# Performance work log

Hardware: AMD Instinct MI355X
Metric: run time of the kernel (lower is better)

## Reference

```python
import jax, jax.numpy as jnp
import numpy as np

N, K, C = 128, 64, 64

def _w(key, shape, scale):
    return (jax.random.normal(key, shape, dtype=jnp.float32) * scale)

def setup_inputs() -> dict:
    key = jax.random.key(0)
    ks = jax.random.split(key, 20)
    s1 = 1.0 / np.sqrt(C)
    s2 = 1.0 / np.sqrt(2 * C)
    inp = {
        "x": jax.random.normal(ks[0], (N, K, C), dtype=jnp.float32),
        "W_lin": _w(ks[1], (C, C), s1), "b_lin": jnp.zeros((C,), jnp.float32),
        # unary_passing: Linear(C,C) -> tanh -> Linear(C,C)
        "Wu1": _w(ks[2], (C, C), s1), "bu1": jnp.zeros((C,), jnp.float32),
        "Wu2": _w(ks[3], (C, C), s1), "bu2": jnp.zeros((C,), jnp.float32),
        # unary_gate: Linear(C,C) -> tanh -> Linear(C,C) -> sigmoid
        "Wug1": _w(ks[4], (C, C), s1), "bug1": jnp.zeros((C,), jnp.float32),
        "Wug2": _w(ks[5], (C, C), s1), "bug2": jnp.zeros((C,), jnp.float32),
        # binary_passing: Linear(2C,C) -> tanh -> Linear(C,C)
        "Wb1": _w(ks[6], (2 * C, C), s2), "bb1": jnp.zeros((C,), jnp.float32),
        "Wb2": _w(ks[7], (C, C), s1), "bb2": jnp.zeros((C,), jnp.float32),
        # binary_gate: Linear(2C,C) -> tanh -> Linear(C,C) -> sigmoid
        "Wbg1": _w(ks[8], (2 * C, C), s2), "bbg1": jnp.zeros((C,), jnp.float32),
        "Wbg2": _w(ks[9], (C, C), s1), "bbg2": jnp.zeros((C,), jnp.float32),
        "t": 0,  # time scalar, ignored by IgnoreLinear base layer
    }
    return inp


def reference(x, W_lin, b_lin, Wu1, bu1, Wu2, bu2, Wug1, bug1, Wug2, bug2,
              Wb1, bb1, Wb2, bb2, Wbg1, bbg1, Wbg2, bbg2, t):
    # base linear map (IgnoreLinear: ignores t)
    h = x @ W_lin + b_lin                          # (N, K, C)
    n, k, c = h.shape
    # unary message with gate
    um = jnp.tanh(h @ Wu1 + bu1) @ Wu2 + bu2
    ug = jax.nn.sigmoid(jnp.tanh(h @ Wug1 + bug1) @ Wug2 + bug2)
    um = um * ug                                   # (N, K, C)
    # all-pairs broadcast-concat: hm[n,i,j] = [h[n,j], h[n,i]]
    hm = jnp.concatenate([
        jnp.broadcast_to(h[:, None, :, :], (n, k, k, c)),
        jnp.broadcast_to(h[:, :, None, :], (n, k, k, c)),
    ], axis=3)                                     # (N, K, K, 2C)
    bm = jnp.tanh(hm @ Wb1 + bb1) @ Wb2 + bb2      # (N, K, K, C)
    bg = jax.nn.sigmoid(jnp.tanh(hm @ Wbg1 + bbg1) @ Wbg2 + bbg2)
    # sum over axis 1 (includes diagonal, as in original), normalize by K-1
    bm = jnp.sum(bm * bg, axis=1) / jnp.float32(k - 1)  # (N, K, C)
    return um + bm
```

## Files before the change

kernel.cpp:

```cpp
#include <hip/hip_runtime.h>

#define WST 72
#define LOG2E 1.44269504f

typedef __attribute__((ext_vector_type(4))) float    f32x4;
typedef __attribute__((ext_vector_type(2))) float    f32x2;
typedef __attribute__((ext_vector_type(8))) _Float16 f16x8;
typedef __attribute__((ext_vector_type(2))) _Float16 f16x2;
typedef __attribute__((ext_vector_type(2))) __fp16   fp16x2_raw;

union U8 { f16x8 v; f16x2 h[4]; };

__device__ __forceinline__ float rcp_f(float x) { return __builtin_amdgcn_rcpf(x); }
__device__ __forceinline__ float exp2_f(float x) { return __builtin_amdgcn_exp2f(x); }
__device__ __forceinline__ float fast_sigmoid(float x) {
    return rcp_f(1.0f + __expf(-x));
}
__device__ __forceinline__ float tanh_exp(float x) {
    return 1.0f - 2.0f * rcp_f(__expf(2.0f * x) + 1.0f);
}
__device__ __forceinline__ f16x2 pkrtz(float a, float b) {
    fp16x2_raw r = __builtin_amdgcn_cvt_pkrtz(a, b);
    return __builtin_bit_cast(f16x2, r);
}

__device__ __forceinline__ void wload8(const float* __restrict__ W, int tid, float v[8]) {
#pragma unroll
    for (int i = 0; i < 8; ++i) v[i] = W[tid + i * 512];
}
__device__ __forceinline__ void wstore8(_Float16* Wt, int tid, const float v[8], float scale) {
#pragma unroll
    for (int i = 0; i < 8; ++i) {
        int idx = tid + i * 512;
        Wt[(idx & 63) * WST + (idx >> 6)] = (_Float16)(v[i] * scale);
    }
}
__device__ __forceinline__ void wload16(const float* __restrict__ W, int t256, float v[16]) {
#pragma unroll
    for (int i = 0; i < 16; ++i) v[i] = W[t256 + i * 256];
}

__device__ __forceinline__ void gemm2(const _Float16* Act, int arow, int qd,
                                      const _Float16* Wt, int colb,
                                      f32x4 acc[2]) {
    f16x8 a0 = *(const f16x8*)(Act + arow * WST + qd * 8);
    f16x8 a1 = *(const f16x8*)(Act + arow * WST + 32 + qd * 8);
#pragma unroll
    for (int cc = 0; cc < 2; ++cc) {
        const _Float16* wr = Wt + (colb + cc * 16) * WST + qd * 8;
        f16x8 b0 = *(const f16x8*)(wr);
        f16x8 b1 = *(const f16x8*)(wr + 32);
        acc[cc] = __builtin_amdgcn_mfma_f32_16x16x32_f16(a0, b0, acc[cc], 0, 0, 0);
        acc[cc] = __builtin_amdgcn_mfma_f32_16x16x32_f16(a1, b1, acc[cc], 0, 0, 0);
    }
}

__global__ __launch_bounds__(512, 2) void fused_all_kernel(
    const float* __restrict__ x,
    const float* __restrict__ W_lin, const float* __restrict__ b_lin,
    const float* __restrict__ Wu1,  const float* __restrict__ bu1,
    const float* __restrict__ Wu2,  const float* __restrict__ bu2,
    const float* __restrict__ Wug1, const float* __restrict__ bug1,
    const float* __restrict__ Wug2, const float* __restrict__ bug2,
    const float* __restrict__ Wb1,  const float* __restrict__ bb1,
    const float* __restrict__ Wb2,  const float* __restrict__ bb2,
    const float* __restrict__ Wbg1, const float* __restrict__ bbg1,
    const float* __restrict__ Wbg2, const float* __restrict__ bbg2,
    float* __restrict__ out)
{
    __shared__ __align__(16) char smem[152576];
    _Float16* WLs = (_Float16*)(smem);
    _Float16* SX  = (_Float16*)(smem + 9216);
    _Float16* SH  = (_Float16*)(smem + 18432);
    _Float16* W1  = (_Float16*)(smem + 27648);
    _Float16* W2  = (_Float16*)(smem + 36864);
    _Float16* W3  = (_Float16*)(smem + 46080);
    _Float16* W4  = (_Float16*)(smem + 55296);
    _Float16* W5  = (_Float16*)(smem + 64512);
    _Float16* W6  = (_Float16*)(smem + 73728);
    _Float16* W7  = (_Float16*)(smem + 82944);
    float*    EPm  = (float*)(smem + 92160);
    float*    EPgm = (float*)(smem + 100864);
    float*    EQb  = (float*)(smem + 109568);
    float*    EQgb = (float*)(smem + 125952);
    float*    um32 = (float*)(smem + 142336);
    float*    csP  = (float*)(smem + 150528);
    float*    Red  = (float*)(smem);

    int tid = threadIdx.x, w = tid >> 6, l = tid & 63;
    int qd = l >> 4, l16 = l & 15;
    int n = blockIdx.x >> 1, jsel = blockIdx.x & 1;

    int rw = w & 3, ch = w >> 2;
    int arow = rw * 16 + l16;
    int colb = ch * 32 + l16;
    int crow = rw * 16 + qd * 4;

    int s = w & 3;
    int lr16 = (s & 1) * 16;
    int cb32 = (s >> 1) * 32;
    bool loW = (w < 4);

    f32x4 acc[2];

#pragma unroll
    for (int i = 0; i < 4; ++i) {
        int e = tid * 2 + i * 1024;
        f32x2 v = *(const f32x2*)(x + (size_t)n * 4096 + e);
        f16x2 p; p[0] = (_Float16)v[0]; p[1] = (_Float16)v[1];
        *(f16x2*)(SX + (e >> 6) * WST + (e & 63)) = p;
    }
    {
        float wv[8];
        wload8(W_lin, tid, wv);
        wstore8(WLs, tid, wv, 1.0f);
    }
    __syncthreads();

    {
        float wv0[8], wv1[8], wv2[8], wv3[8], wv4[8], wv5[8];
        wload8(Wb1, tid, wv0);
        wload8(Wb1 + 4096, tid, wv1);
        wload8(Wbg1, tid, wv2);
        wload8(Wbg1 + 4096, tid, wv3);
        wload8(Wu1, tid, wv4);
        wload8(Wug1, tid, wv5);
#pragma unroll
        for (int cc = 0; cc < 2; ++cc) {
            float bv = b_lin[colb + cc * 16];
            acc[cc] = (f32x4){bv, bv, bv, bv};
        }
        gemm2(SX, arow, qd, WLs, colb, acc);
#pragma unroll
        for (int cc = 0; cc < 2; ++cc)
#pragma unroll
            for (int r = 0; r < 4; ++r)
                SH[(crow + r) * WST + colb + cc * 16] = (_Float16)acc[cc][r];
        wstore8(W1, tid, wv0, 1.0f);
        wstore8(W2, tid, wv1, 1.0f);
        wstore8(W3, tid, wv2, 1.0f);
        wstore8(W4, tid, wv3, 1.0f);
        wstore8(W5, tid, wv4, 1.0f);
        wstore8(W6, tid, wv5, 1.0f);
    }
    __syncthreads();

    {
        float wu2v[8], wug2v[8];
        wload8(Wu2, tid, wu2v);
        wload8(Wug2, tid, wug2v);

        acc[0] = (f32x4){0.f, 0.f, 0.f, 0.f};
        acc[1] = (f32x4){0.f, 0.f, 0.f, 0.f};
        gemm2(SH, arow, qd, W2, colb, acc);
#pragma unroll
        for (int cc = 0; cc < 2; ++cc)
#pragma unroll
            for (int r = 0; r < 4; ++r)
                EQb[(crow + r) * 64 + colb + cc * 16] = __expf(2.0f * acc[cc][r]);

        f32x4 accg[2];
        accg[0] = (f32x4){0.f, 0.f, 0.f, 0.f};
        accg[1] = (f32x4){0.f, 0.f, 0.f, 0.f};
        gemm2(SH, arow, qd, W4, colb, accg);
#pragma unroll
        for (int cc = 0; cc < 2; ++cc)
#pragma unroll
            for (int r = 0; r < 4; ++r)
                EQgb[(crow + r) * 64 + colb + cc * 16] = __expf(2.0f * accg[cc][r]);

        const _Float16* Wp = loW ? W1 : W3;
        const _Float16* Wt = loW ? W5 : W6;
        const float* bp = loW ? bb1 : bbg1;
        const float* bt = loW ? bu1 : bug1;
        float* EPdst = loW ? EPm : EPgm;
        _Float16* Tdst = loW ? WLs : (WLs + 2304);

        f32x4 accp[2];
#pragma unroll
        for (int cc = 0; cc < 2; ++cc) {
            float bv = bp[cb32 + cc * 16 + l16];
            accp[cc] = (f32x4){bv, bv, bv, bv};
        }
        gemm2(SH, jsel * 32 + lr16 + l16, qd, Wp, cb32 + l16, accp);
#pragma unroll
        for (int cc = 0; cc < 2; ++cc)
#pragma unroll
            for (int r = 0; r < 4; ++r)
                EPdst[(lr16 + qd * 4 + r) * 68 + cb32 + cc * 16 + l16] =
                    __expf(2.0f * accp[cc][r]);

        f32x4 acct[2];
#pragma unroll
        for (int cc = 0; cc < 2; ++cc) {
            float bv = bt[cb32 + cc * 16 + l16];
            acct[cc] = (f32x4){bv, bv, bv, bv};
        }
        gemm2(SH, jsel * 32 + lr16 + l16, qd, Wt, cb32 + l16, acct);
#pragma unroll
        for (int cc = 0; cc < 2; ++cc)
#pragma unroll
            for (int r = 0; r < 4; ++r)
                Tdst[(lr16 + qd * 4 + r) * WST + cb32 + cc * 16 + l16] =
                    (_Float16)tanh_exp(acct[cc][r]);

        wstore8(SX, tid, wu2v, 1.0f);
        wstore8(W7, tid, wug2v, 1.0f);
    }
    __syncthreads();

    if (loW) {
        f32x4 ua[2], ga[2];
#pragma unroll
        for (int cc = 0; cc < 2; ++cc) {
            float bv = bu2[cb32 + cc * 16 + l16];
            ua[cc] = (f32x4){bv, bv, bv, bv};
        }
        gemm2(WLs, lr16 + l16, qd, SX, cb32 + l16, ua);
#pragma unroll
        for (int cc = 0; cc < 2; ++cc) {
            float bv = bug2[cb32 + cc * 16 + l16];
            ga[cc] = (f32x4){bv, bv, bv, bv};
        }
        gemm2(WLs + 2304, lr16 + l16, qd, W7, cb32 + l16, ga);
#pragma unroll
        for (int cc = 0; cc < 2; ++cc)
#pragma unroll
            for (int r = 0; r < 4; ++r)
                um32[(lr16 + qd * 4 + r) * 64 + cb32 + cc * 16 + l16] =
                    ua[cc][r] * fast_sigmoid(ga[cc][r]);
    } else {
        int tid2 = tid - 256;
        float wm[16], wg[16];
        wload16(Wb2, tid2, wm);
        wload16(Wbg2, tid2, wg);
        float csm = 0.0f, csg = 0.0f;
#pragma unroll
        for (int i = 0; i < 16; ++i) {
            int idx = tid2 + i * 256;
            int o = (idx & 63) * WST + (idx >> 6);
            _Float16 a = (_Float16)(wm[i] * -2.0f);
            _Float16 b = (_Float16)(wg[i] * (2.0f * LOG2E));
            W1[o] = a;
            W2[o] = b;
            csm += (float)a;
            csg += (float)b;
        }
        int q = tid2 >> 6, c = tid2 & 63;
        csP[q * 64 + c] = csm;
        csP[256 + q * 64 + c] = csg;
    }
    __syncthreads();

    int jgrp = w >> 2, iw = w & 3;

    f16x8 bwm[4][2], bwg[4][2];
#pragma unroll
    for (int cc = 0; cc < 4; ++cc)
#pragma unroll
        for (int kk = 0; kk < 2; ++kk) {
            bwm[cc][kk] = *(const f16x8*)(W1 + (cc * 16 + l16) * WST + kk * 32 + qd * 8);
            bwg[cc][kk] = *(const f16x8*)(W2 + (cc * 16 + l16) * WST + kk * 32 + qd * 8);
        }
    float bim[4], big[4];
#pragma unroll
    for (int cc = 0; cc < 4; ++cc) {
        int c = cc * 16 + l16;
        bim[cc] = bb2[c] -
            0.5f * (csP[c] + csP[64 + c] + csP[128 + c] + csP[192 + c]);
        big[cc] = -LOG2E * bbg2[c] -
            0.5f * (csP[256 + c] + csP[320 + c] + csP[384 + c] + csP[448 + c]);
    }

    const float* pr  = EPm  + (jgrp * 16 + l16) * 68;
    const float* pgr = EPgm + (jgrp * 16 + l16) * 68;
    f32x4 pm[4], pg[4];
    pm[0] = *(const f32x4*)(pr + qd * 8);
    pm[1] = *(const f32x4*)(pr + qd * 8 + 4);
    pm[2] = *(const f32x4*)(pr + 32 + qd * 8);
    pm[3] = *(const f32x4*)(pr + 32 + qd * 8 + 4);
    pg[0] = *(const f32x4*)(pgr + qd * 8);
    pg[1] = *(const f32x4*)(pgr + qd * 8 + 4);
    pg[2] = *(const f32x4*)(pgr + 32 + qd * 8);
    pg[3] = *(const f32x4*)(pgr + 32 + qd * 8 + 4);

    f32x4 bacc[4];
#pragma unroll
    for (int cc = 0; cc < 4; ++cc) bacc[cc] = (f32x4){0.f, 0.f, 0.f, 0.f};

    for (int ii = iw * 16; ii < iw * 16 + 16; ++ii) {
        const float* qm = EQb  + ii * 64;
        const float* qg = EQgb + ii * 64;
        U8 am[2], ag[2];
#pragma unroll
        for (int kk = 0; kk < 2; ++kk) {
            int cb = kk * 32 + qd * 8;
            f32x4 qa = *(const f32x4*)(qm + cb);
            f32x4 qb = *(const f32x4*)(qm + cb + 4);
            f32x4 ha = *(const f32x4*)(qg + cb);
            f32x4 hb = *(const f32x4*)(qg + cb + 4);
#pragma unroll
            for (int t = 0; t < 2; ++t) {
                float a0 = __builtin_fmaf(pm[kk*2][2*t],   qa[2*t],   1.0f);
                float a1 = __builtin_fmaf(pm[kk*2][2*t+1], qa[2*t+1], 1.0f);
                float ri = rcp_f(a0 * a1);
                am[kk].h[t]     = pkrtz(ri * a1, ri * a0);
                float b0f = __builtin_fmaf(pm[kk*2+1][2*t],   qb[2*t],   1.0f);
                float b1f = __builtin_fmaf(pm[kk*2+1][2*t+1], qb[2*t+1], 1.0f);
                float rj = rcp_f(b0f * b1f);
                am[kk].h[2 + t] = pkrtz(rj * b1f, rj * b0f);
                float c0 = __builtin_fmaf(pg[kk*2][2*t],   ha[2*t],   1.0f);
                float c1 = __builtin_fmaf(pg[kk*2][2*t+1], ha[2*t+1], 1.0f);
                float rk = rcp_f(c0 * c1);
                ag[kk].h[t]     = pkrtz(rk * c1, rk * c0);
                float d0 = __builtin_fmaf(pg[kk*2+1][2*t],   hb[2*t],   1.0f);
                float d1 = __builtin_fmaf(pg[kk*2+1][2*t+1], hb[2*t+1], 1.0f);
                float rl = rcp_f(d0 * d1);
                ag[kk].h[2 + t] = pkrtz(rl * d1, rl * d0);
            }
        }
#pragma unroll
        for (int cc = 0; cc < 4; ++cc) {
            f32x4 d = {bim[cc], bim[cc], bim[cc], bim[cc]};
            d = __builtin_amdgcn_mfma_f32_16x16x32_f16(am[0].v, bwm[cc][0], d, 0, 0, 0);
            d = __builtin_amdgcn_mfma_f32_16x16x32_f16(am[1].v, bwm[cc][1], d, 0, 0, 0);
            f32x4 e = {big[cc], big[cc], big[cc], big[cc]};
            e = __builtin_amdgcn_mfma_f32_16x16x32_f16(ag[0].v, bwg[cc][0], e, 0, 0, 0);
            e = __builtin_amdgcn_mfma_f32_16x16x32_f16(ag[1].v, bwg[cc][1], e, 0, 0, 0);
            float v0 = exp2_f(e[0]), v1 = exp2_f(e[1]);
            float u0 = 1.0f + v0, u1 = 1.0f + v1;
            float r01 = rcp_f(u0 * u1);
            bacc[cc][0] = __builtin_fmaf(d[0] * u1, r01, bacc[cc][0]);
            bacc[cc][1] = __builtin_fmaf(d[1] * u0, r01, bacc[cc][1]);
            float v2 = exp2_f(e[2]), v3 = exp2_f(e[3]);
            float u2 = 1.0f + v2, u3 = 1.0f + v3;
            float r23 = rcp_f(u2 * u3);
            bacc[cc][2] = __builtin_fmaf(d[2] * u3, r23, bacc[cc][2]);
            bacc[cc][3] = __builtin_fmaf(d[3] * u2, r23, bacc[cc][3]);
        }
    }

    __syncthreads();
#pragma unroll
    for (int cc = 0; cc < 4; ++cc)
#pragma unroll
        for (int r = 0; r < 4; ++r)
            Red[(jgrp * 4 + iw) * 1024 + (qd * 4 + r) * 64 + cc * 16 + l16] = bacc[cc][r];
    __syncthreads();

    {
        int e = tid * 4;
        int lr = e >> 6, col = e & 63;
        int g = lr >> 4, rr = lr & 15;
        f32x4 sv = {0.f, 0.f, 0.f, 0.f};
#pragma unroll
        for (int p = 0; p < 4; ++p)
            sv += *(const f32x4*)(Red + (g * 4 + p) * 1024 + rr * 64 + col);
        f32x4 u = *(const f32x4*)(um32 + lr * 64 + col);
        f32x4 o;
#pragma unroll
        for (int t = 0; t < 4; ++t)
            o[t] = u[t] + sv[t] * (1.0f / 63.0f);
        *(f32x4*)(out + (size_t)n * 4096 + (size_t)(jsel * 32 + lr) * 64 + col) = o;
    }
}

extern "C" void kernel_launch(void* const* d_in, const int* in_sizes, int n_in,
                              void* d_out, int out_size, void* d_ws, size_t ws_size,
                              hipStream_t stream)
{
    (void)in_sizes; (void)n_in; (void)out_size; (void)d_ws; (void)ws_size;
    const float* x     = (const float*)d_in[0];
    const float* W_lin = (const float*)d_in[1];
    const float* b_lin = (const float*)d_in[2];
    const float* Wu1   = (const float*)d_in[3];
    const float* bu1   = (const float*)d_in[4];
    const float* Wu2   = (const float*)d_in[5];
    const float* bu2   = (const float*)d_in[6];
    const float* Wug1  = (const float*)d_in[7];
    const float* bug1  = (const float*)d_in[8];
    const float* Wug2  = (const float*)d_in[9];
    const float* bug2  = (const float*)d_in[10];
    const float* Wb1   = (const float*)d_in[11];
    const float* bb1   = (const float*)d_in[12];
    const float* Wb2   = (const float*)d_in[13];
    const float* bb2   = (const float*)d_in[14];
    const float* Wbg1  = (const float*)d_in[15];
    const float* bbg1  = (const float*)d_in[16];
    const float* Wbg2  = (const float*)d_in[17];
    const float* bbg2  = (const float*)d_in[18];

    hipLaunchKernelGGL(fused_all_kernel, dim3(256), dim3(512), 0, stream,
        x, W_lin, b_lin, Wu1, bu1, Wu2, bu2, Wug1, bug1, Wug2, bug2,
        Wb1, bb1, Wb2, bb2, Wbg1, bbg1, Wbg2, bbg2,
        (float*)d_out);
}
```

Baseline: 117.4 us.

## Shrink LDS footprint by reusing buffers and reading small weights straight from global

Cuts the shared memory per block from about 149KB to about 77KB by staging the binary weights in two phases that reuse the same buffers and by aliasing the EP, um and reduction buffers. The unary and second-layer weights are now read directly from global memory into MFMA fragments instead of being staged in LDS. Column sums are computed with wave shuffles. The launch bound is raised so two blocks can fit per CU. In exchange there are more barriers, serialized GEMM phases, and uncoalesced strided global reads for the weight fragments.

```diff
diff --git a/kernel.cpp b/kernel.cpp
--- a/kernel.cpp
+++ b/kernel.cpp
@@ -28,16 +28,43 @@
 #pragma unroll
     for (int i = 0; i < 8; ++i) v[i] = W[tid + i * 512];
 }
-__device__ __forceinline__ void wstore8(_Float16* Wt, int tid, const float v[8], float scale) {
+__device__ __forceinline__ void wstore8(_Float16* Wt, int tid, const float v[8]) {
 #pragma unroll
     for (int i = 0; i < 8; ++i) {
         int idx = tid + i * 512;
-        Wt[(idx & 63) * WST + (idx >> 6)] = (_Float16)(v[i] * scale);
-    }
-}
-__device__ __forceinline__ void wload16(const float* __restrict__ W, int t256, float v[16]) {
-#pragma unroll
-    for (int i = 0; i < 16; ++i) v[i] = W[t256 + i * 256];
+        Wt[(idx & 63) * WST + (idx >> 6)] = (_Float16)v[i];
+    }
+}
+
+__device__ __forceinline__ void gfrag(const float* __restrict__ W, int col,
+                                      int qd, float scale, f16x8& b0, f16x8& b1) {
+#pragma unroll
+    for (int t = 0; t < 8; ++t) {
+        b0[t] = (_Float16)(W[(qd * 8 + t) * 64 + col] * scale);
+        b1[t] = (_Float16)(W[(32 + qd * 8 + t) * 64 + col] * scale);
+    }
+}
+
+__device__ __forceinline__ void gemm1(const _Float16* Act, int arow, int qd,
+                                      const _Float16* Wt, int bcol, f32x4& acc) {
+    f16x8 a0 = *(const f16x8*)(Act + arow * WST + qd * 8);
+    f16x8 a1 = *(const f16x8*)(Act + arow * WST + 32 + qd * 8);
+    const _Float16* wr = Wt + bcol * WST + qd * 8;
+    f16x8 b0 = *(const f16x8*)(wr);
+    f16x8 b1 = *(const f16x8*)(wr + 32);
+    acc = __builtin_amdgcn_mfma_f32_16x16x32_f16(a0, b0, acc, 0, 0, 0);
+    acc = __builtin_amdgcn_mfma_f32_16x16x32_f16(a1, b1, acc, 0, 0, 0);
+}
+
+__device__ __forceinline__ void gemm1g(const _Float16* Act, int arow, int qd,
+                                       const float* __restrict__ W, int bcol,
+                                       f32x4& acc) {
+    f16x8 a0 = *(const f16x8*)(Act + arow * WST + qd * 8);
+    f16x8 a1 = *(const f16x8*)(Act + arow * WST + 32 + qd * 8);
+    f16x8 b0, b1;
+    gfrag(W, bcol, qd, 1.0f, b0, b1);
+    acc = __builtin_amdgcn_mfma_f32_16x16x32_f16(a0, b0, acc, 0, 0, 0);
+    acc = __builtin_amdgcn_mfma_f32_16x16x32_f16(a1, b1, acc, 0, 0, 0);
 }
 
 __device__ __forceinline__ void gemm2(const _Float16* Act, int arow, int qd,
@@ -55,7 +82,7 @@
     }
 }
 
-__global__ __launch_bounds__(512, 2) void fused_all_kernel(
+__global__ __launch_bounds__(512, 4) void fused_all_kernel(
     const float* __restrict__ x,
     const float* __restrict__ W_lin, const float* __restrict__ b_lin,
     const float* __restrict__ Wu1,  const float* __restrict__ bu1,
@@ -68,24 +95,18 @@
     const float* __restrict__ Wbg2, const float* __restrict__ bbg2,
     float* __restrict__ out)
 {
-    __shared__ __align__(16) char smem[152576];
-    _Float16* WLs = (_Float16*)(smem);
-    _Float16* SX  = (_Float16*)(smem + 9216);
-    _Float16* SH  = (_Float16*)(smem + 18432);
-    _Float16* W1  = (_Float16*)(smem + 27648);
-    _Float16* W2  = (_Float16*)(smem + 36864);
-    _Float16* W3  = (_Float16*)(smem + 46080);
-    _Float16* W4  = (_Float16*)(smem + 55296);
-    _Float16* W5  = (_Float16*)(smem + 64512);
-    _Float16* W6  = (_Float16*)(smem + 73728);
-    _Float16* W7  = (_Float16*)(smem + 82944);
-    float*    EPm  = (float*)(smem + 92160);
-    float*    EPgm = (float*)(smem + 100864);
-    float*    EQb  = (float*)(smem + 109568);
-    float*    EQgb = (float*)(smem + 125952);
-    float*    um32 = (float*)(smem + 142336);
-    float*    csP  = (float*)(smem + 150528);
-    float*    Red  = (float*)(smem);
+    __shared__ __align__(16) char smem[78848];
+    _Float16* A   = (_Float16*)(smem);
+    _Float16* B   = (_Float16*)(smem + 9216);
+    _Float16* C   = (_Float16*)(smem + 18432);
+    _Float16* D   = (_Float16*)(smem + 27648);
+    _Float16* SH  = (_Float16*)(smem + 36864);
+    float*    EQb  = (float*)(smem + 46080);
+    float*    EQgb = (float*)(smem + 62464);
+    float*    EPm  = (float*)(smem);
+    float*    EPgm = (float*)(smem + 9216);
+    float*    um   = (float*)(smem + 27648);
+    float*    Red  = (float*)(smem + 46080);
 
     int tid = threadIdx.x, w = tid >> 6, l = tid & 63;
     int qd = l >> 4, l16 = l & 15;
@@ -96,10 +117,10 @@
     int colb = ch * 32 + l16;
     int crow = rw * 16 + qd * 4;
 
-    int s = w & 3;
-    int lr16 = (s & 1) * 16;
-    int cb32 = (s >> 1) * 32;
-    bool loW = (w < 4);
+    int rh = w & 1, cq = w >> 1;
+    int srow = rh * 16 + l16;
+    int scol = cq * 16 + l16;
+    int scrow = rh * 16 + qd * 4;
 
     f32x4 acc[2];
 
@@ -108,169 +129,127 @@
         int e = tid * 2 + i * 1024;
         f32x2 v = *(const f32x2*)(x + (size_t)n * 4096 + e);
         f16x2 p; p[0] = (_Float16)v[0]; p[1] = (_Float16)v[1];
-        *(f16x2*)(SX + (e >> 6) * WST + (e & 63)) = p;
+        *(f16x2*)(A + (e >> 6) * WST + (e & 63)) = p;
     }
     {
         float wv[8];
         wload8(W_lin, tid, wv);
-        wstore8(WLs, tid, wv, 1.0f);
-    }
-    __syncthreads();
-
-    {
-        float wv0[8], wv1[8], wv2[8], wv3[8], wv4[8], wv5[8];
-        wload8(Wb1, tid, wv0);
-        wload8(Wb1 + 4096, tid, wv1);
-        wload8(Wbg1, tid, wv2);
-        wload8(Wbg1 + 4096, tid, wv3);
-        wload8(Wu1, tid, wv4);
-        wload8(Wug1, tid, wv5);
+        wstore8(B, tid, wv);
+    }
+    __syncthreads();
+
+    {
+        float wvP[8], wvQ[8];
+        wload8(Wb1, tid, wvP);
+        wload8(Wb1 + 4096, tid, wvQ);
 #pragma unroll
         for (int cc = 0; cc < 2; ++cc) {
             float bv = b_lin[colb + cc * 16];
             acc[cc] = (f32x4){bv, bv, bv, bv};
         }
-        gemm2(SX, arow, qd, WLs, colb, acc);
+        gemm2(A, arow, qd, B, colb, acc);
 #pragma unroll
         for (int cc = 0; cc < 2; ++cc)
 #pragma unroll
             for (int r = 0; r < 4; ++r)
                 SH[(crow + r) * WST + colb + cc * 16] = (_Float16)acc[cc][r];
-        wstore8(W1, tid, wv0, 1.0f);
-        wstore8(W2, tid, wv1, 1.0f);
-        wstore8(W3, tid, wv2, 1.0f);
-        wstore8(W4, tid, wv3, 1.0f);
-        wstore8(W5, tid, wv4, 1.0f);
-        wstore8(W6, tid, wv5, 1.0f);
-    }
-    __syncthreads();
-
-    {
-        float wu2v[8], wug2v[8];
-        wload8(Wu2, tid, wu2v);
-        wload8(Wug2, tid, wug2v);
-
-        acc[0] = (f32x4){0.f, 0.f, 0.f, 0.f};
-        acc[1] = (f32x4){0.f, 0.f, 0.f, 0.f};
-        gemm2(SH, arow, qd, W2, colb, acc);
-#pragma unroll
-        for (int cc = 0; cc < 2; ++cc)
-#pragma unroll
-            for (int r = 0; r < 4; ++r)
-                EQb[(crow + r) * 64 + colb + cc * 16] = __expf(2.0f * acc[cc][r]);
-
-        f32x4 accg[2];
-        accg[0] = (f32x4){0.f, 0.f, 0.f, 0.f};
-        accg[1] = (f32x4){0.f, 0.f, 0.f, 0.f};
-        gemm2(SH, arow, qd, W4, colb, accg);
-#pragma unroll
-        for (int cc = 0; cc < 2; ++cc)
-#pragma unroll
-            for (int r = 0; r < 4; ++r)
-                EQgb[(crow + r) * 64 + colb + cc * 16] = __expf(2.0f * accg[cc][r]);
-
-        const _Float16* Wp = loW ? W1 : W3;
-        const _Float16* Wt = loW ? W5 : W6;
-        const float* bp = loW ? bb1 : bbg1;
-        const float* bt = loW ? bu1 : bug1;
-        float* EPdst = loW ? EPm : EPgm;
-        _Float16* Tdst = loW ? WLs : (WLs + 2304);
-
-        f32x4 accp[2];
-#pragma unroll
-        for (int cc = 0; cc < 2; ++cc) {
-            float bv = bp[cb32 + cc * 16 + l16];
-            accp[cc] = (f32x4){bv, bv, bv, bv};
+        wstore8(C, tid, wvP);
+        wstore8(D, tid, wvQ);
+    }
+    __syncthreads();
+
+    float wvP[8], wvQ[8];
+    wload8(Wbg1, tid, wvP);
+    wload8(Wbg1 + 4096, tid, wvQ);
+    acc[0] = (f32x4){0.f, 0.f, 0.f, 0.f};
+    acc[1] = (f32x4){0.f, 0.f, 0.f, 0.f};
+    gemm2(SH, arow, qd, D, colb, acc);
+#pragma unroll
+    for (int cc = 0; cc < 2; ++cc)
+#pragma unroll
+        for (int r = 0; r < 4; ++r)
+            EQb[(crow + r) * 64 + colb + cc * 16] = __expf(2.0f * acc[cc][r]);
+    {
+        float bv = bb1[scol];
+        f32x4 ap = (f32x4){bv, bv, bv, bv};
+        gemm1(SH, jsel * 32 + srow, qd, C, scol, ap);
+#pragma unroll
+        for (int r = 0; r < 4; ++r)
+            EPm[(scrow + r) * 68 + scol] = __expf(2.0f * ap[r]);
+    }
+    __syncthreads();
+
+    f32x4 accu, accg;
+    {
+        wstore8(C, tid, wvP);
+        wstore8(D, tid, wvQ);
+        float bv = bu1[scol];
+        accu = (f32x4){bv, bv, bv, bv};
+        gemm1g(SH, jsel * 32 + srow, qd, Wu1, scol, accu);
+        bv = bug1[scol];
+        accg = (f32x4){bv, bv, bv, bv};
+        gemm1g(SH, jsel * 32 + srow, qd, Wug1, scol, accg);
+    }
+    __syncthreads();
+
+    acc[0] = (f32x4){0.f, 0.f, 0.f, 0.f};
+    acc[1] = (f32x4){0.f, 0.f, 0.f, 0.f};
+    gemm2(SH, arow, qd, D, colb, acc);
+#pragma unroll
+    for (int cc = 0; cc < 2; ++cc)
+#pragma unroll
+        for (int r = 0; r < 4; ++r)
+            EQgb[(crow + r) * 64 + colb + cc * 16] = __expf(2.0f * acc[cc][r]);
+    {
+        float bv = bbg1[scol];
+        f32x4 ap = (f32x4){bv, bv, bv, bv};
+        gemm1(SH, jsel * 32 + srow, qd, C, scol, ap);
+#pragma unroll
+        for (int r = 0; r < 4; ++r)
+            EPgm[(scrow + r) * 68 + scol] = __expf(2.0f * ap[r]);
+    }
+    __syncthreads();
+
+#pragma unroll
+    for (int r = 0; r < 4; ++r) {
+        SH[(scrow + r) * WST + scol] = (_Float16)tanh_exp(accu[r]);
+        SH[(32 + scrow + r) * WST + scol] = (_Float16)tanh_exp(accg[r]);
+    }
+    __syncthreads();
+
+    f16x8 bwm[4][2], bwg[4][2];
+    float bim[4], big[4];
+    {
+        float bv = bu2[scol];
+        f32x4 ua = (f32x4){bv, bv, bv, bv};
+        gemm1g(SH, srow, qd, Wu2, scol, ua);
+        bv = bug2[scol];
+        f32x4 ga = (f32x4){bv, bv, bv, bv};
+        gemm1g(SH, 32 + srow, qd, Wug2, scol, ga);
+#pragma unroll
+        for (int r = 0; r < 4; ++r)
+            um[(scrow + r) * 64 + scol] = ua[r] * fast_sigmoid(ga[r]);
+
+#pragma unroll
+        for (int cc = 0; cc < 4; ++cc) {
+            int c = cc * 16 + l16;
+            gfrag(Wb2, c, qd, -2.0f, bwm[cc][0], bwm[cc][1]);
+            gfrag(Wbg2, c, qd, 2.0f * LOG2E, bwg[cc][0], bwg[cc][1]);
+            float sm = 0.0f, sg = 0.0f;
+#pragma unroll
+            for (int t = 0; t < 8; ++t) {
+                sm += (float)bwm[cc][0][t] + (float)bwm[cc][1][t];
+                sg += (float)bwg[cc][0][t] + (float)bwg[cc][1][t];
+            }
+            sm += __shfl_xor(sm, 16); sm += __shfl_xor(sm, 32);
+            sg += __shfl_xor(sg, 16); sg += __shfl_xor(sg, 32);
+            bim[cc] = bb2[c] - 0.5f * sm;
+            big[cc] = -LOG2E * bbg2[c] - 0.5f * sg;
         }
-        gemm2(SH, jsel * 32 + lr16 + l16, qd, Wp, cb32 + l16, accp);
-#pragma unroll
-        for (int cc = 0; cc < 2; ++cc)
-#pragma unroll
-            for (int r = 0; r < 4; ++r)
-                EPdst[(lr16 + qd * 4 + r) * 68 + cb32 + cc * 16 + l16] =
-                    __expf(2.0f * accp[cc][r]);
-
-        f32x4 acct[2];
-#pragma unroll
-        for (int cc = 0; cc < 2; ++cc) {
-            float bv = bt[cb32 + cc * 16 + l16];
-            acct[cc] = (f32x4){bv, bv, bv, bv};
-        }
-        gemm2(SH, jsel * 32 + lr16 + l16, qd, Wt, cb32 + l16, acct);
-#pragma unroll
-        for (int cc = 0; cc < 2; ++cc)
-#pragma unroll
-            for (int r = 0; r < 4; ++r)
-                Tdst[(lr16 + qd * 4 + r) * WST + cb32 + cc * 16 + l16] =
-                    (_Float16)tanh_exp(acct[cc][r]);
-
-        wstore8(SX, tid, wu2v, 1.0f);
-        wstore8(W7, tid, wug2v, 1.0f);
-    }
-    __syncthreads();
-
-    if (loW) {
-        f32x4 ua[2], ga[2];
-#pragma unroll
-        for (int cc = 0; cc < 2; ++cc) {
-            float bv = bu2[cb32 + cc * 16 + l16];
-            ua[cc] = (f32x4){bv, bv, bv, bv};
-        }
-        gemm2(WLs, lr16 + l16, qd, SX, cb32 + l16, ua);
-#pragma unroll
-        for (int cc = 0; cc < 2; ++cc) {
-            float bv = bug2[cb32 + cc * 16 + l16];
-            ga[cc] = (f32x4){bv, bv, bv, bv};
-        }
-        gemm2(WLs + 2304, lr16 + l16, qd, W7, cb32 + l16, ga);
-#pragma unroll
-        for (int cc = 0; cc < 2; ++cc)
-#pragma unroll
-            for (int r = 0; r < 4; ++r)
-                um32[(lr16 + qd * 4 + r) * 64 + cb32 + cc * 16 + l16] =
-                    ua[cc][r] * fast_sigmoid(ga[cc][r]);
-    } else {
-        int tid2 = tid - 256;
-        float wm[16], wg[16];
-        wload16(Wb2, tid2, wm);
-        wload16(Wbg2, tid2, wg);
-        float csm = 0.0f, csg = 0.0f;
-#pragma unroll
-        for (int i = 0; i < 16; ++i) {
-            int idx = tid2 + i * 256;
-            int o = (idx & 63) * WST + (idx >> 6);
-            _Float16 a = (_Float16)(wm[i] * -2.0f);
-            _Float16 b = (_Float16)(wg[i] * (2.0f * LOG2E));
-            W1[o] = a;
-            W2[o] = b;
-            csm += (float)a;
-            csg += (float)b;
-        }
-        int q = tid2 >> 6, c = tid2 & 63;
-        csP[q * 64 + c] = csm;
-        csP[256 + q * 64 + c] = csg;
     }
     __syncthreads();
 
     int jgrp = w >> 2, iw = w & 3;
-
-    f16x8 bwm[4][2], bwg[4][2];
-#pragma unroll
-    for (int cc = 0; cc < 4; ++cc)
-#pragma unroll
-        for (int kk = 0; kk < 2; ++kk) {
-            bwm[cc][kk] = *(const f16x8*)(W1 + (cc * 16 + l16) * WST + kk * 32 + qd * 8);
-            bwg[cc][kk] = *(const f16x8*)(W2 + (cc * 16 + l16) * WST + kk * 32 + qd * 8);
-        }
-    float bim[4], big[4];
-#pragma unroll
-    for (int cc = 0; cc < 4; ++cc) {
-        int c = cc * 16 + l16;
-        bim[cc] = bb2[c] -
-            0.5f * (csP[c] + csP[64 + c] + csP[128 + c] + csP[192 + c]);
-        big[cc] = -LOG2E * bbg2[c] -
-            0.5f * (csP[256 + c] + csP[320 + c] + csP[384 + c] + csP[448 + c]);
-    }
 
     const float* pr  = EPm  + (jgrp * 16 + l16) * 68;
     const float* pgr = EPgm + (jgrp * 16 + l16) * 68;
@@ -356,7 +335,7 @@
 #pragma unroll
         for (int p = 0; p < 4; ++p)
             sv += *(const f32x4*)(Red + (g * 4 + p) * 1024 + rr * 64 + col);
-        f32x4 u = *(const f32x4*)(um32 + lr * 64 + col);
+        f32x4 u = *(const f32x4*)(um + lr * 64 + col);
         f32x4 o;
 #pragma unroll
         for (int t = 0; t < 4; ++t)
```

New measurement: 158.9 us. 35.4% more time.
